# Kernel optimization log

Measured on AMD Instinct MI355X. Metric: run time of the kernel, lower is better.

The kernel has to match this reference:

```python
import math
import jax, jax.numpy as jnp
import numpy as np

WH, WW = 7, 7
NUM_HEADS = 16


def _relative_position_index(wh, ww):
    # Static int index table, identical to the torch buffer construction.
    ch, cw = np.arange(wh), np.arange(ww)
    coords = np.stack(np.meshgrid(ch, cw, indexing='ij'))        # (2, wh, ww)
    cf = coords.reshape(2, -1)                                    # (2, N)
    rel = cf[:, :, None] - cf[:, None, :]                         # (2, N, N)
    rel = rel.transpose(1, 2, 0).copy()                           # (N, N, 2)
    rel[:, :, 0] += wh - 1
    rel[:, :, 1] += ww - 1
    rel[:, :, 0] *= 2 * ww - 1
    return rel.sum(-1)                                            # (N, N) int


def setup_inputs() -> dict:
    key = jax.random.key(0)
    ks = jax.random.split(key, 7)
    B_, N, C = 2048, WH * WW, 512
    nW = 64
    s = 1.0 / math.sqrt(C)
    return {
        'x': jax.random.normal(ks[0], (B_, N, C), jnp.float32),
        'mask': jax.random.normal(ks[1], (nW, N, N), jnp.float32),
        'qkv_w': jax.random.normal(ks[2], (3 * C, C), jnp.float32) * s,
        'qkv_b': jax.random.normal(ks[3], (3 * C,), jnp.float32) * 0.02,
        'proj_w': jax.random.normal(ks[4], (C, C), jnp.float32) * s,
        'proj_b': jax.random.normal(ks[5], (C,), jnp.float32) * 0.02,
        'bias_table': jax.random.normal(ks[6], (2 * WH - 1, 2 * WW - 1, NUM_HEADS), jnp.float32) * 0.02,
    }


def reference(x, mask, qkv_w, qkv_b, proj_w, proj_b, bias_table):
    B_, N, C = x.shape
    nH = NUM_HEADS
    hd = C // nH
    scale = math.sqrt(hd)  # self.scale = qk_scale or sqrt(head_dim)

    qkv = x @ qkv_w.T + qkv_b                                   # (B_, N, 3C)
    qkv = qkv.reshape(B_, N, 3, nH, hd).transpose(2, 0, 3, 1, 4)  # (3, B_, nH, N, hd)
    q, k, v = qkv[0], qkv[1], qkv[2]

    attn = jnp.einsum('bhnd,bhmd->bhnm', q, k) / scale           # (B_, nH, N, N)

    idx = _relative_position_index(WH, WW).reshape(-1)            # (N*N,) static
    bias = bias_table.reshape(-1, nH)[idx].reshape(N, N, nH)      # gather
    attn = attn + bias.transpose(2, 0, 1)[None]                   # (B_, nH, N, N)

    nW = mask.shape[0]
    attn = attn.reshape(B_ // nW, nW, nH, N, N) + mask[None, :, None]
    attn = attn.reshape(B_, nH, N, N)

    attn = jax.nn.softmax(attn, axis=-1)
    out = jnp.einsum('bhnm,bhmd->bhnd', attn, v)                  # (B_, nH, N, hd)
    out = out.transpose(0, 2, 1, 3).reshape(B_, N, C)
    return out @ proj_w.T + proj_b
```

## Files before the change

kernel.cpp:

```cpp
#include <hip/hip_runtime.h>
#include <hip/hip_bf16.h>


typedef __bf16  bf16x8 __attribute__((ext_vector_type(8)));
typedef float   f32x4  __attribute__((ext_vector_type(4)));

#define B_TOT   2048
#define NTOK    49
#define CDIM    512
#define NHEAD   16
#define HDIM    32
#define MROWS   (B_TOT * NTOK)
#define QKVN    (3 * CDIM)

__device__ __forceinline__ void load_lds16(const void* gptr, void* lptr) {
    __builtin_amdgcn_global_load_lds(
        (const __attribute__((address_space(1))) unsigned int*)gptr,
        (__attribute__((address_space(3))) unsigned int*)lptr,
        16, 0, 0);
}
__device__ __forceinline__ void load_lds4(const void* gptr, void* lptr) {
    __builtin_amdgcn_global_load_lds(
        (const __attribute__((address_space(1))) unsigned int*)gptr,
        (__attribute__((address_space(3))) unsigned int*)lptr,
        4, 0, 0);
}

__global__ void cvt_f32_bf16(const float* __restrict__ in,
                             __hip_bfloat16* __restrict__ out, int n4) {
    int idx = blockIdx.x * blockDim.x + threadIdx.x;
    int stride = gridDim.x * blockDim.x;
    for (int i = idx; i < n4; i += stride) {
        float4 f = ((const float4*)in)[i];
        union { __hip_bfloat16 h[4]; ushort4 u; } c;
        c.h[0] = __float2bfloat16(f.x);
        c.h[1] = __float2bfloat16(f.y);
        c.h[2] = __float2bfloat16(f.z);
        c.h[3] = __float2bfloat16(f.w);
        ((ushort4*)out)[i] = c.u;
    }
}

#define BARR    asm volatile("s_barrier" ::: "memory")
#define WAITV(N) asm volatile("s_waitcnt vmcnt(" #N ")" ::: "memory")
#define MFMA16(av, bv, cv) __builtin_amdgcn_mfma_f32_16x16x32_bf16(av, bv, cv, 0, 0, 0)

template <typename OutT>
__global__ __launch_bounds__(512, 2) void gemm256(
    const __hip_bfloat16* __restrict__ A,
    const __hip_bfloat16* __restrict__ B,
    const float* __restrict__ bias,
    OutT* __restrict__ C,
    int M, int N, int K, int nbx, int cpx)
{
    extern __shared__ __align__(16) char smem[];
    char* sA = smem;
    char* sB = smem + 65536;

    const int NT = K >> 6;

    const int tid  = threadIdx.x;
    const int lane = tid & 63;
    const int wave = tid >> 6;
    const int wm   = wave >> 2;
    const int wn   = wave & 3;
    const int l16  = lane & 15;
    const int quad = lane >> 4;

    const int id = blockIdx.x;
    const int sw = (id & 7) * cpx + (id >> 3);
    const int mb = sw / nbx;
    const int nb = sw - mb * nbx;
    const int m0 = mb << 8;
    const int n0 = nb << 8;

    const int r  = tid >> 2;
    const int ch = tid & 3;
    const __hip_bfloat16* Ag0 = A + (size_t)(m0 + r) * K + ch * 8;
    const __hip_bfloat16* Ag1 = Ag0 + (size_t)128 * K;
    const __hip_bfloat16* Bg0 = B + (size_t)(n0 + r) * K + ch * 8;
    const __hip_bfloat16* Bg1 = Bg0 + (size_t)128 * K;
    char* dA = sA + tid * 16;
    char* dB = sB + tid * 16;

#define STAGE_A(t2, kh) \
    { load_lds16(Ag0 + (t2) * 64 + (kh) * 32, dA + ((t2) & 1) * 32768 + (kh) * 16384);        \
      load_lds16(Ag1 + (t2) * 64 + (kh) * 32, dA + ((t2) & 1) * 32768 + (kh) * 16384 + 8192); }
#define STAGE_B(t2, kh) \
    { load_lds16(Bg0 + (t2) * 64 + (kh) * 32, dB + ((t2) & 1) * 32768 + (kh) * 16384);        \
      load_lds16(Bg1 + (t2) * 64 + (kh) * 32, dB + ((t2) & 1) * 32768 + (kh) * 16384 + 8192); }

    STAGE_A(0, 0); STAGE_B(0, 0);
    STAGE_A(0, 1); STAGE_B(0, 1);
    STAGE_A(1, 0); STAGE_B(1, 0);
    WAITV(8);
    BARR;

    const int tA = (wm * 128 + l16) * 64 + quad * 16;
    const int tB = (wn * 64  + l16) * 64 + quad * 16;

    f32x4 acc[8][4] = {};
    bf16x8 a[8], b[2];

#pragma unroll 2
    for (int t = 0; t < NT; ++t) {
        const int sl = (t & 1) * 32768;
        const char* pA0 = sA + sl;
        const char* pB0 = sB + sl;
        const char* pA1 = sA + sl + 16384;
        const char* pB1 = sB + sl + 16384;

#pragma unroll
        for (int i = 0; i < 8; ++i) a[i] = *(const bf16x8*)(pA0 + tA + i * 1024);
        b[0] = *(const bf16x8*)(pB0 + tB);
        b[1] = *(const bf16x8*)(pB0 + tB + 1024);
        if (t + 1 < NT) STAGE_A(t + 1, 1);
        BARR;
        __builtin_amdgcn_s_setprio(1);
#pragma unroll
        for (int i = 0; i < 8; ++i) {
            acc[i][0] = MFMA16(a[i], b[0], acc[i][0]);
            acc[i][1] = MFMA16(a[i], b[1], acc[i][1]);
        }
        __builtin_amdgcn_s_setprio(0);
        BARR;

        b[0] = *(const bf16x8*)(pB0 + tB + 2048);
        b[1] = *(const bf16x8*)(pB0 + tB + 3072);
        if (t + 1 < NT) STAGE_B(t + 1, 1);
        BARR;
        __builtin_amdgcn_s_setprio(1);
#pragma unroll
        for (int i = 0; i < 8; ++i) {
            acc[i][2] = MFMA16(a[i], b[0], acc[i][2]);
            acc[i][3] = MFMA16(a[i], b[1], acc[i][3]);
        }
        __builtin_amdgcn_s_setprio(0);
        if (t < NT - 1) { WAITV(8); } else { WAITV(0); }
        BARR;

#pragma unroll
        for (int i = 0; i < 8; ++i) a[i] = *(const bf16x8*)(pA1 + tA + i * 1024);
        b[0] = *(const bf16x8*)(pB1 + tB);
        b[1] = *(const bf16x8*)(pB1 + tB + 1024);
        if (t + 2 < NT) STAGE_A(t + 2, 0);
        BARR;
        __builtin_amdgcn_s_setprio(1);
#pragma unroll
        for (int i = 0; i < 8; ++i) {
            acc[i][0] = MFMA16(a[i], b[0], acc[i][0]);
            acc[i][1] = MFMA16(a[i], b[1], acc[i][1]);
        }
        __builtin_amdgcn_s_setprio(0);
        BARR;

        b[0] = *(const bf16x8*)(pB1 + tB + 2048);
        b[1] = *(const bf16x8*)(pB1 + tB + 3072);
        if (t + 2 < NT) STAGE_B(t + 2, 0);
        BARR;
        __builtin_amdgcn_s_setprio(1);
#pragma unroll
        for (int i = 0; i < 8; ++i) {
            acc[i][2] = MFMA16(a[i], b[0], acc[i][2]);
            acc[i][3] = MFMA16(a[i], b[1], acc[i][3]);
        }
        __builtin_amdgcn_s_setprio(0);
        if (t < NT - 2) { WAITV(8); }
        else if (t == NT - 2) { WAITV(4); }
        BARR;
    }
#undef STAGE_A
#undef STAGE_B

#pragma unroll
    for (int i = 0; i < 8; ++i) {
#pragma unroll
        for (int jj = 0; jj < 4; ++jj) {
            const int col = n0 + wn * 64 + jj * 16 + l16;
            const float bv = bias[col];
#pragma unroll
            for (int rr = 0; rr < 4; ++rr) {
                const int row = m0 + wm * 128 + i * 16 + quad * 4 + rr;
                const float val = acc[i][jj][rr] + bv;
                if constexpr (sizeof(OutT) == 2)
                    C[(size_t)row * N + col] = __float2bfloat16(val);
                else
                    C[(size_t)row * N + col] = val;
            }
        }
    }
}

#define QS_OFF   0
#define KS_OFF   12544
#define VS_OFF   25088
#define BIAS_OFF 41472
#define MASK_OFF 42824
#define SMEM_BYTES 52432

__global__ __launch_bounds__(256) void attn_mfma(
    const __hip_bfloat16* __restrict__ qkv,
    const float* __restrict__ mask,
    const float* __restrict__ bias_table,
    __hip_bfloat16* __restrict__ out)
{
    __shared__ __align__(16) char smem[SMEM_BYTES];

    const int tid  = threadIdx.x;
    const int lane = tid & 63;
    const int w    = tid >> 6;
    const int l16  = lane & 15;
    const int quad = lane >> 4;
    const int b    = blockIdx.x >> 2;
    const int hq   = blockIdx.x & 3;

    {
        const long rowbase = (long)b * NTOK * QKVN;
        for (int e = tid; e < 2352; e += 256) {
            const int m   = e / 784;
            const int rr  = e - m * 784;
            const int tok = rr >> 4, seg = rr & 15;
            const int segl = seg ^ (tok & 7);
            const __hip_bfloat16* src =
                qkv + rowbase + (long)tok * QKVN + m * 512 + hq * 128 + segl * 8;
            load_lds16(src, smem + e * 16);
        }
        for (int e = tid; e < 960; e += 256)
            ((unsigned int*)(smem + VS_OFF + 49 * 256))[e] = 0u;
        const float* msrc = mask + (long)(b & 63) * (NTOK * NTOK);
        for (int e = tid; e < NTOK * NTOK; e += 256)
            load_lds4(msrc + e, smem + MASK_OFF + e * 4);
        __hip_bfloat16* sb = (__hip_bfloat16*)(smem + BIAS_OFF);
        for (int e = tid; e < 676; e += 256) {
            const int w2 = e / 169, rel = e - w2 * 169;
            sb[e] = __float2bfloat16(bias_table[rel * NHEAD + hq * 4 + w2]);
        }
    }
    __syncthreads();

    const int fro = (w * 64 + quad * 16) ^ ((l16 & 7) << 4);
    bf16x8 af[4], bf[4];
#pragma unroll
    for (int t = 0; t < 4; ++t) {
        const int tok = t * 16 + l16;
        af[t] = *(const bf16x8*)(smem + KS_OFF + tok * 256 + fro);
        bf[t] = *(const bf16x8*)(smem + QS_OFF + tok * 256 + fro);
    }
    f32x4 acc[4][4] = {};
#pragma unroll
    for (int i = 0; i < 4; ++i)
#pragma unroll
        for (int j = 0; j < 4; ++j)
            acc[i][j] = __builtin_amdgcn_mfma_f32_16x16x32_bf16(
                af[i], bf[j], acc[i][j], 0, 0, 0);
    __syncthreads();

    const float scale = 0.17677669529663687f;
    const float* smf = (const float*)(smem + MASK_OFF);
    const __hip_bfloat16* sb = (const __hip_bfloat16*)(smem + BIAS_OFF);
    const int quad4 = quad * 4;

    int kp[4][4];
#pragma unroll
    for (int i = 0; i < 4; ++i)
#pragma unroll
        for (int r = 0; r < 4; ++r) {
            const int k  = i * 16 + quad4 + r;
            const int rj = k / 7, cj = k - rj * 7;
            kp[i][r] = (6 - rj) * 13 + (6 - cj);
        }

    char* pbase = smem + w * 6272;
#pragma unroll
    for (int j = 0; j < 4; ++j) {
        const int q   = j * 16 + l16;
        const bool qok = q < NTOK;
        const int ri  = q / 7, ci = q - ri * 7;
        const int qp  = ri * 13 + ci;
        const int mrow = q * NTOK;
        float mx = -1e30f;
#pragma unroll
        for (int i = 0; i < 4; ++i)
#pragma unroll
            for (int r = 0; r < 4; ++r) {
                const int k = i * 16 + quad4 + r;
                float v;
                if (qok && k < NTOK) {
                    v = fmaf(acc[i][j][r], scale,
                             __bfloat162float(sb[w * 169 + qp + kp[i][r]]) + smf[mrow + k]);
                } else {
                    v = -1e30f;
                }
                acc[i][j][r] = v;
                mx = fmaxf(mx, v);
            }
        mx = fmaxf(mx, __shfl_xor(mx, 16));
        mx = fmaxf(mx, __shfl_xor(mx, 32));
        float s = 0.f;
#pragma unroll
        for (int i = 0; i < 4; ++i)
#pragma unroll
            for (int r = 0; r < 4; ++r) {
                const float ev = __expf(acc[i][j][r] - mx);
                acc[i][j][r] = ev;
                s += ev;
            }
        s += __shfl_xor(s, 16);
        s += __shfl_xor(s, 32);
        const float inv = 1.0f / s;
        if (qok) {
            char* prow = pbase + q * 128;
            const int xr = (q & 7) << 4;
#pragma unroll
            for (int i = 0; i < 4; ++i) {
                union { __hip_bfloat16 h[4]; uint2 u; } pk;
#pragma unroll
                for (int r = 0; r < 4; ++r)
                    pk.h[r] = __float2bfloat16(acc[i][j][r] * inv);
                *(uint2*)(prow + ((i * 32 + quad * 8) ^ xr)) = pk.u;
            }
        }
    }
    __syncthreads();

    bf16x8 pa[4][2];
#pragma unroll
    for (int mt = 0; mt < 4; ++mt) {
        const int q  = mt * 16 + l16;
        const int xr = (q & 7) << 4;
#pragma unroll
        for (int ks = 0; ks < 2; ++ks)
            pa[mt][ks] = *(const bf16x8*)(pbase + q * 128 + ((ks * 64 + quad * 16) ^ xr));
    }
    bf16x8 vb[2][2];
#pragma unroll
    for (int dt = 0; dt < 2; ++dt)
#pragma unroll
        for (int ks = 0; ks < 2; ++ks)
#pragma unroll
            for (int e = 0; e < 8; ++e) {
                const int key = ks * 32 + quad * 8 + e;
                const int dby = (w * 32 + dt * 16 + l16) * 2;
                vb[dt][ks][e] = *(const __bf16*)(smem + VS_OFF + key * 256 + (dby ^ (e << 4)));
            }
    f32x4 o[4][2] = {};
#pragma unroll
    for (int mt = 0; mt < 4; ++mt)
#pragma unroll
        for (int dt = 0; dt < 2; ++dt)
#pragma unroll
            for (int ks = 0; ks < 2; ++ks)
                o[mt][dt] = __builtin_amdgcn_mfma_f32_16x16x32_bf16(
                    pa[mt][ks], vb[dt][ks], o[mt][dt], 0, 0, 0);

    const long obase = (long)b * NTOK * CDIM + hq * 128 + w * 32;
#pragma unroll
    for (int mt = 0; mt < 4; ++mt)
#pragma unroll
        for (int r = 0; r < 4; ++r) {
            const int q = mt * 16 + quad4 + r;
            if (q < NTOK) {
                const long rb = obase + (long)q * CDIM;
#pragma unroll
                for (int dt = 0; dt < 2; ++dt)
                    out[rb + dt * 16 + l16] = __float2bfloat16(o[mt][dt][r]);
            }
        }
}

extern "C" void kernel_launch(void* const* d_in, const int* in_sizes, int n_in,
                              void* d_out, int out_size, void* d_ws, size_t ws_size,
                              hipStream_t stream) {
    const float* x          = (const float*)d_in[0];
    const float* mask       = (const float*)d_in[1];
    const float* qkv_w      = (const float*)d_in[2];
    const float* qkv_b      = (const float*)d_in[3];
    const float* proj_w     = (const float*)d_in[4];
    const float* proj_b     = (const float*)d_in[5];
    const float* bias_table = (const float*)d_in[6];

    char* ws = (char*)d_ws;
    __hip_bfloat16* xb   = (__hip_bfloat16*)(ws);
    __hip_bfloat16* qw   = (__hip_bfloat16*)(ws + 102760448);
    __hip_bfloat16* pw   = (__hip_bfloat16*)(ws + 104333312);
    __hip_bfloat16* qkvb = (__hip_bfloat16*)(ws + 104857600);
    __hip_bfloat16* ao   = xb;

    static int attr_done = 0;
    if (!attr_done) {
        hipFuncSetAttribute(
            reinterpret_cast<const void*>(&gemm256<__hip_bfloat16>),
            hipFuncAttributeMaxDynamicSharedMemorySize, 131072);
        hipFuncSetAttribute(
            reinterpret_cast<const void*>(&gemm256<float>),
            hipFuncAttributeMaxDynamicSharedMemorySize, 131072);
        attr_done = 1;
    }

    cvt_f32_bf16<<<32768, 256, 0, stream>>>(x, xb, (MROWS * CDIM) / 4);
    cvt_f32_bf16<<<768,   256, 0, stream>>>(qkv_w, qw, (QKVN * CDIM) / 4);
    cvt_f32_bf16<<<256,   256, 0, stream>>>(proj_w, pw, (CDIM * CDIM) / 4);

    gemm256<__hip_bfloat16><<<2352, 512, 131072, stream>>>(
        xb, qw, qkv_b, qkvb, MROWS, QKVN, CDIM, 6, 294);

    attn_mfma<<<B_TOT * 4, 256, 0, stream>>>(qkvb, mask, bias_table, ao);

    gemm256<float><<<784, 512, 131072, stream>>>(
        ao, pw, proj_b, (float*)d_out, MROWS, CDIM, CDIM, 2, 98);
}
```

Measured before the change: 774.2 us.

## Restructure GEMM main loop with XOR-swizzled LDS layout and fewer barriers

```diff
diff --git a/kernel.cpp b/kernel.cpp
--- a/kernel.cpp
+++ b/kernel.cpp
@@ -74,103 +74,95 @@
     const int m0 = mb << 8;
     const int n0 = nb << 8;
 
-    const int r  = tid >> 2;
-    const int ch = tid & 3;
-    const __hip_bfloat16* Ag0 = A + (size_t)(m0 + r) * K + ch * 8;
-    const __hip_bfloat16* Ag1 = Ag0 + (size_t)128 * K;
-    const __hip_bfloat16* Bg0 = B + (size_t)(n0 + r) * K + ch * 8;
-    const __hip_bfloat16* Bg1 = Bg0 + (size_t)128 * K;
-    char* dA = sA + tid * 16;
-    char* dB = sB + tid * 16;
-
-#define STAGE_A(t2, kh) \
-    { load_lds16(Ag0 + (t2) * 64 + (kh) * 32, dA + ((t2) & 1) * 32768 + (kh) * 16384);        \
-      load_lds16(Ag1 + (t2) * 64 + (kh) * 32, dA + ((t2) & 1) * 32768 + (kh) * 16384 + 8192); }
-#define STAGE_B(t2, kh) \
-    { load_lds16(Bg0 + (t2) * 64 + (kh) * 32, dB + ((t2) & 1) * 32768 + (kh) * 16384);        \
-      load_lds16(Bg1 + (t2) * 64 + (kh) * 32, dB + ((t2) & 1) * 32768 + (kh) * 16384 + 8192); }
-
-    STAGE_A(0, 0); STAGE_B(0, 0);
-    STAGE_A(0, 1); STAGE_B(0, 1);
-    STAGE_A(1, 0); STAGE_B(1, 0);
+    const int srow = tid >> 3;
+    const int scg  = ((tid & 7) << 3) ^ ((srow & 7) << 3);
+    const __hip_bfloat16* Asrc = A + (size_t)(m0 + srow) * K + scg;
+    const __hip_bfloat16* Bsrc = B + (size_t)(n0 + srow) * K + scg;
+    char* dAl = sA + tid * 16;
+    char* dBl = sB + tid * 16;
+
+#define STG_A(t2, h) \
+    { load_lds16(Asrc + (size_t)(h) * 128 * K + (t2) * 64,            \
+                 dAl + ((t2) & 1) * 32768 + (h) * 16384);             \
+      load_lds16(Asrc + ((size_t)(h) * 128 + 64) * K + (t2) * 64,     \
+                 dAl + ((t2) & 1) * 32768 + (h) * 16384 + 8192); }
+#define STG_B(t2, h) \
+    { load_lds16(Bsrc + (size_t)(h) * 128 * K + (t2) * 64,            \
+                 dBl + ((t2) & 1) * 32768 + (h) * 16384);             \
+      load_lds16(Bsrc + ((size_t)(h) * 128 + 64) * K + (t2) * 64,     \
+                 dBl + ((t2) & 1) * 32768 + (h) * 16384 + 8192); }
+
+    STG_A(0, 0); STG_A(0, 1); STG_B(0, 0); STG_B(0, 1);
+    STG_A(1, 0); STG_A(1, 1); STG_B(1, 0); STG_B(1, 1);
     WAITV(8);
     BARR;
 
-    const int tA = (wm * 128 + l16) * 64 + quad * 16;
-    const int tB = (wn * 64  + l16) * 64 + quad * 16;
+    const int c0 = (quad * 16) ^ ((l16 & 7) << 4);
+    const int c1 = c0 ^ 64;
 
     f32x4 acc[8][4] = {};
-    bf16x8 a[8], b[2];
+
+#define CLUSTER(mfa, mfb)                                                  \
+    {                                                                      \
+        bf16x8 xk0 = *(const bf16x8*)(pA + (mfa) * 2048 + c0);             \
+        bf16x8 xk1 = *(const bf16x8*)(pA + (mfa) * 2048 + c1);             \
+        bf16x8 yk0 = *(const bf16x8*)(pA + (mfb) * 2048 + c0);             \
+        bf16x8 yk1 = *(const bf16x8*)(pA + (mfb) * 2048 + c1);             \
+        __builtin_amdgcn_s_setprio(1);                                     \
+        _Pragma("unroll")                                                  \
+        for (int nf = 0; nf < 4; ++nf) {                                   \
+            acc[mfa][nf] = MFMA16(xk0, Bf0[nf], acc[mfa][nf]);             \
+            acc[mfa][nf] = MFMA16(xk1, Bf1[nf], acc[mfa][nf]);             \
+            acc[mfb][nf] = MFMA16(yk0, Bf0[nf], acc[mfb][nf]);             \
+            acc[mfb][nf] = MFMA16(yk1, Bf1[nf], acc[mfb][nf]);             \
+        }                                                                  \
+        __builtin_amdgcn_s_setprio(0);                                     \
+    }
 
 #pragma unroll 2
     for (int t = 0; t < NT; ++t) {
         const int sl = (t & 1) * 32768;
-        const char* pA0 = sA + sl;
-        const char* pB0 = sB + sl;
-        const char* pA1 = sA + sl + 16384;
-        const char* pB1 = sB + sl + 16384;
-
-#pragma unroll
-        for (int i = 0; i < 8; ++i) a[i] = *(const bf16x8*)(pA0 + tA + i * 1024);
-        b[0] = *(const bf16x8*)(pB0 + tB);
-        b[1] = *(const bf16x8*)(pB0 + tB + 1024);
-        if (t + 1 < NT) STAGE_A(t + 1, 1);
+        const char* pA = sA + sl + wm * 16384 + l16 * 128;
+        const char* pB = sB + sl + (wn >> 1) * 16384 + ((wn & 1) * 64 + l16) * 128;
+
+        bf16x8 Bf0[4], Bf1[4];
+#pragma unroll
+        for (int nf = 0; nf < 4; ++nf) {
+            Bf0[nf] = *(const bf16x8*)(pB + nf * 2048 + c0);
+            Bf1[nf] = *(const bf16x8*)(pB + nf * 2048 + c1);
+        }
+
+        CLUSTER(0, 1);
+        CLUSTER(2, 3);
+        CLUSTER(4, 5);
+
+        bf16x8 a6k0 = *(const bf16x8*)(pA + 6 * 2048 + c0);
+        bf16x8 a6k1 = *(const bf16x8*)(pA + 6 * 2048 + c1);
+        bf16x8 a7k0 = *(const bf16x8*)(pA + 7 * 2048 + c0);
+        bf16x8 a7k1 = *(const bf16x8*)(pA + 7 * 2048 + c1);
+        asm volatile("s_waitcnt lgkmcnt(0)" ::: "memory");
         BARR;
+
+        if (t + 2 < NT) { STG_A(t + 2, 0); STG_A(t + 2, 1);
+                          STG_B(t + 2, 0); STG_B(t + 2, 1); }
+
         __builtin_amdgcn_s_setprio(1);
 #pragma unroll
-        for (int i = 0; i < 8; ++i) {
-            acc[i][0] = MFMA16(a[i], b[0], acc[i][0]);
-            acc[i][1] = MFMA16(a[i], b[1], acc[i][1]);
+        for (int nf = 0; nf < 4; ++nf) {
+            acc[6][nf] = MFMA16(a6k0, Bf0[nf], acc[6][nf]);
+            acc[6][nf] = MFMA16(a6k1, Bf1[nf], acc[6][nf]);
+            acc[7][nf] = MFMA16(a7k0, Bf0[nf], acc[7][nf]);
+            acc[7][nf] = MFMA16(a7k1, Bf1[nf], acc[7][nf]);
         }
         __builtin_amdgcn_s_setprio(0);
+
+        if (t + 2 < NT) { WAITV(8); }
+        else if (t + 1 < NT) { WAITV(0); }
         BARR;
-
-        b[0] = *(const bf16x8*)(pB0 + tB + 2048);
-        b[1] = *(const bf16x8*)(pB0 + tB + 3072);
-        if (t + 1 < NT) STAGE_B(t + 1, 1);
-        BARR;
-        __builtin_amdgcn_s_setprio(1);
-#pragma unroll
-        for (int i = 0; i < 8; ++i) {
-            acc[i][2] = MFMA16(a[i], b[0], acc[i][2]);
-            acc[i][3] = MFMA16(a[i], b[1], acc[i][3]);
-        }
-        __builtin_amdgcn_s_setprio(0);
-        if (t < NT - 1) { WAITV(8); } else { WAITV(0); }
-        BARR;
-
-#pragma unroll
-        for (int i = 0; i < 8; ++i) a[i] = *(const bf16x8*)(pA1 + tA + i * 1024);
-        b[0] = *(const bf16x8*)(pB1 + tB);
-        b[1] = *(const bf16x8*)(pB1 + tB + 1024);
-        if (t + 2 < NT) STAGE_A(t + 2, 0);
-        BARR;
-        __builtin_amdgcn_s_setprio(1);
-#pragma unroll
-        for (int i = 0; i < 8; ++i) {
-            acc[i][0] = MFMA16(a[i], b[0], acc[i][0]);
-            acc[i][1] = MFMA16(a[i], b[1], acc[i][1]);
-        }
-        __builtin_amdgcn_s_setprio(0);
-        BARR;
-
-        b[0] = *(const bf16x8*)(pB1 + tB + 2048);
-        b[1] = *(const bf16x8*)(pB1 + tB + 3072);
-        if (t + 2 < NT) STAGE_B(t + 2, 0);
-        BARR;
-        __builtin_amdgcn_s_setprio(1);
-#pragma unroll
-        for (int i = 0; i < 8; ++i) {
-            acc[i][2] = MFMA16(a[i], b[0], acc[i][2]);
-            acc[i][3] = MFMA16(a[i], b[1], acc[i][3]);
-        }
-        __builtin_amdgcn_s_setprio(0);
-        if (t < NT - 2) { WAITV(8); }
-        else if (t == NT - 2) { WAITV(4); }
-        BARR;
-    }
-#undef STAGE_A
-#undef STAGE_B
+    }
+#undef CLUSTER
+#undef STG_A
+#undef STG_B
 
 #pragma unroll
     for (int i = 0; i < 8; ++i) {
```

New measurement: 754.2 us. 1.03x faster.
